# Optimization experiments

Hardware: AMD Instinct MI355X
Metric: run time of the kernel (lower is better)

Reference implementation:

```python
import jax, jax.numpy as jnp
import numpy as np

GAMMA = 0.997
N_STEPS = 5
EPS = 1e-3
Q_WEIGHTS = np.array([1.0, 0.5, 0.0, 2.0], dtype=np.float32)


def _rescale(x):
    # sign(x) * (sqrt(|x|+1) - 1) + eps * x
    return jnp.sign(x) * (jnp.sqrt(jnp.abs(x) + 1.0) - 1.0) + EPS * x


def _inv_rescale(x):
    sign = jnp.sign(x)
    sqrt_arg = 1.0 + 4.0 * EPS * (jnp.abs(x) + 1.0 + EPS)
    square = ((jnp.sqrt(sqrt_arg) - 1.0) / (2.0 * EPS)) ** 2
    return sign * (square - 1.0)


def setup_inputs() -> dict:
    key = jax.random.key(0)
    ks = jax.random.split(key, 6)
    B, T, Q = 4096, 512, 4
    current_q_value = jax.random.normal(ks[0], (B, T, Q), dtype=jnp.float32)
    next_q_value = jax.random.normal(ks[1], (B, T, Q), dtype=jnp.float32)
    log_p = jax.random.normal(ks[2], (B, T), dtype=jnp.float32)
    reward = jax.random.normal(ks[3], (B, T, Q), dtype=jnp.float32)
    is_done = jax.random.bernoulli(ks[4], 0.02, (B, T)).astype(jnp.float32)
    mask = jax.random.bernoulli(ks[5], 0.95, (B, T)).astype(jnp.float32)
    return {
        "current_q_value": current_q_value,
        "next_q_value": next_q_value,
        "log_p": log_p,
        "reward": reward,
        "is_done": is_done,
        "mask": mask,
    }


def reference(current_q_value, next_q_value, log_p, reward, is_done, mask):
    B, T, Q = reward.shape
    q_w = jnp.asarray(Q_WEIGHTS)[None, None, :]                     # (1,1,Q)
    nz = (q_w != 0)
    inv_qw = jnp.where(nz, 1.0 / jnp.where(nz, q_w, 1.0), 0.0)      # (1,1,Q)
    inv_num_q = 1.0 / float((Q_WEIGHTS != 0).sum())

    m = mask[..., None]                                             # (B,T,1)
    d = is_done[..., None]                                          # (B,T,1)

    nq = m * (1.0 - d) * _inv_rescale(next_q_value)                 # (B,T,Q)
    lp = inv_num_q * inv_qw * (m * (1.0 - d) * log_p[..., None])    # (B,T,Q)

    pad = jnp.zeros((B, N_STEPS - 1, Q), dtype=reward.dtype)
    pad_reward = jnp.concatenate([m * reward, pad], axis=1)         # (B,T+n-1,Q)
    lp_pad = jnp.concatenate([lp, pad], axis=1)                     # (B,T+n-1,Q)

    gpow = GAMMA ** jnp.arange(N_STEPS, dtype=jnp.float32)          # gamma^0..gamma^{n-1}
    widx = jnp.arange(T)[:, None] + jnp.arange(N_STEPS)[None, :]    # (T,n) window indices

    reward_sum = jnp.einsum('btnq,n->btq', pad_reward[:, widx, :], gpow)
    log_p_sum = jnp.einsum('btnq,n->btq', lp_pad[:, widx, :], gpow * GAMMA)

    idxs = jnp.minimum(T - 1, jnp.arange(T) + N_STEPS - 1)          # (T,)
    # NOTE: original code uses gamma**idx (absolute index), reproduced faithfully
    next_term = (GAMMA ** idxs.astype(jnp.float32))[None, :, None] * nq[:, idxs, :]

    target = _rescale(reward_sum + next_term + log_p_sum)           # (B,T,Q)
    loss = 0.5 * m * q_w * (current_q_value - target) ** 2
    return loss
```

## Files before the change

kernel.cpp:

```cpp
#include <hip/hip_runtime.h>
#include <math.h>

#define T_DIM 512
#define GAMMA_F 0.997f
#define EPS_F 1e-3f
#define LOG2_GAMMA (-0.0043345907f)

typedef float v4f __attribute__((ext_vector_type(4)));

__device__ __forceinline__ float inv_rescale_f(float x) {
    float s = (x > 0.f) ? 1.f : ((x < 0.f) ? -1.f : 0.f);
    float sqrt_arg = 1.f + 4.f * EPS_F * (fabsf(x) + 1.f + EPS_F);
    float q = (sqrtf(sqrt_arg) - 1.f) * (1.f / (2.f * EPS_F));
    return s * (q * q - 1.f);
}

__device__ __forceinline__ float rescale_f(float x) {
    return copysignf(sqrtf(fabsf(x) + 1.f) - 1.f, x) + EPS_F * x;
}

__global__ __launch_bounds__(256) void nstep_qloss_kernel(
    const float* __restrict__ cur_q,
    const float* __restrict__ next_q,
    const float* __restrict__ log_p,
    const float* __restrict__ reward,
    const float* __restrict__ is_done,
    const float* __restrict__ mask,
    float* __restrict__ out,
    int BT)
{
    int idx = blockIdx.x * 256 + threadIdx.x;
    if (idx >= BT) return;
    int t = idx & (T_DIM - 1);
    int base = idx - t;

    int s1 = (t + 1 < T_DIM) ? t + 1 : T_DIM - 1;
    int s2 = (t + 2 < T_DIM) ? t + 2 : T_DIM - 1;
    int s3 = (t + 3 < T_DIM) ? t + 3 : T_DIM - 1;
    int s4 = (t + 4 < T_DIM) ? t + 4 : T_DIM - 1;
    int o0 = idx;
    int o1 = base + s1, o2 = base + s2, o3 = base + s3, o4 = base + s4;

    const v4f* rew4 = (const v4f*)reward;
    const v4f* nq4  = (const v4f*)next_q;
    const v4f* cq4  = (const v4f*)cur_q;
    v4f* out4       = (v4f*)out;

    float m0 = mask[o0], m1 = mask[o1], m2 = mask[o2], m3 = mask[o3], m4 = mask[o4];
    float d0 = is_done[o0], d1 = is_done[o1], d2 = is_done[o2], d3 = is_done[o3], d4 = is_done[o4];
    float p0 = log_p[o0], p1 = log_p[o1], p2 = log_p[o2], p3 = log_p[o3], p4 = log_p[o4];
    v4f r0 = rew4[o0], r1 = rew4[o1], r2 = rew4[o2], r3 = rew4[o3], r4 = rew4[o4];
    v4f nq = nq4[o4];
    v4f cq = cq4[o0];

    float v1 = (t + 1 < T_DIM) ? 1.f : 0.f;
    float v2 = (t + 2 < T_DIM) ? 1.f : 0.f;
    float v3 = (t + 3 < T_DIM) ? 1.f : 0.f;
    float v4v = (t + 4 < T_DIM) ? 1.f : 0.f;

    const float g1 = GAMMA_F;
    const float g2 = g1 * g1;
    const float g3 = g2 * g1;
    const float g4 = g2 * g2;

    float w0 = m0;
    float w1 = v1 * g1 * m1;
    float w2 = v2 * g2 * m2;
    float w3 = v3 * g3 * m3;
    float w4 = v4v * g4 * m4;

    float a0 = w0 * r0.x; float a1 = w0 * r0.y; float a2 = w0 * r0.z; float a3 = w0 * r0.w;
    a0 = fmaf(w1, r1.x, a0); a1 = fmaf(w1, r1.y, a1); a2 = fmaf(w1, r1.z, a2); a3 = fmaf(w1, r1.w, a3);
    a0 = fmaf(w2, r2.x, a0); a1 = fmaf(w2, r2.y, a1); a2 = fmaf(w2, r2.z, a2); a3 = fmaf(w2, r2.w, a3);
    a0 = fmaf(w3, r3.x, a0); a1 = fmaf(w3, r3.y, a1); a2 = fmaf(w3, r3.z, a2); a3 = fmaf(w3, r3.w, a3);
    a0 = fmaf(w4, r4.x, a0); a1 = fmaf(w4, r4.y, a1); a2 = fmaf(w4, r4.z, a2); a3 = fmaf(w4, r4.w, a3);

    float Ls = w0 * (1.f - d0) * p0;
    Ls = fmaf(w1, (1.f - d1) * p1, Ls);
    Ls = fmaf(w2, (1.f - d2) * p2, Ls);
    Ls = fmaf(w3, (1.f - d3) * p3, Ls);
    Ls = fmaf(w4, (1.f - d4) * p4, Ls);
    Ls *= GAMMA_F * (1.f / 3.f);

    float coeff = exp2f((float)s4 * LOG2_GAMMA);
    float g = coeff * m4 * (1.f - d4);
    float nt0 = g * inv_rescale_f(nq.x);
    float nt1 = g * inv_rescale_f(nq.y);
    float nt2 = g * inv_rescale_f(nq.z);
    float nt3 = g * inv_rescale_f(nq.w);

    float tgt0 = rescale_f(a0 + nt0 + 1.0f * Ls);
    float tgt1 = rescale_f(a1 + nt1 + 2.0f * Ls);
    float tgt2 = rescale_f(a2 + nt2);
    float tgt3 = rescale_f(a3 + nt3 + 0.5f * Ls);

    float hm = 0.5f * m0;
    float e0 = cq.x - tgt0;
    float e1 = cq.y - tgt1;
    float e3 = cq.w - tgt3;
    (void)tgt2;
    v4f o;
    o.x = hm * e0 * e0;
    o.y = hm * 0.5f * e1 * e1;
    o.z = 0.f;
    o.w = hm * 2.0f * e3 * e3;
    out4[idx] = o;
}

extern "C" void kernel_launch(void* const* d_in, const int* in_sizes, int n_in,
                              void* d_out, int out_size, void* d_ws, size_t ws_size,
                              hipStream_t stream) {
    const float* cur_q   = (const float*)d_in[0];
    const float* next_q  = (const float*)d_in[1];
    const float* log_p   = (const float*)d_in[2];
    const float* reward  = (const float*)d_in[3];
    const float* is_done = (const float*)d_in[4];
    const float* mask    = (const float*)d_in[5];
    float* out = (float*)d_out;

    int BT = in_sizes[2];
    int blocks = (BT + 255) / 256;
    hipLaunchKernelGGL(nstep_qloss_kernel, dim3(blocks), dim3(256), 0, stream,
                       cur_q, next_q, log_p, reward, is_done, mask, out, BT);
}
```

Measured before the change: 157.7 us.

## Share n-step window values via wave shuffles and process two elements per thread

Each lane now loads only its own mask, done flag, log_p and reward, then gathers the four following timesteps from neighbouring lanes with shuffle-down instead of issuing five overlapping loads. Waves advance by 60 elements so the last four lanes act as a halo, and each thread handles one element from each half of the flattened B*T range to expose more memory-level parallelism. This is meant to cut redundant global and cache load traffic. In exchange it adds shuffle instructions and about 6% of lanes that compute but never store.

```diff
diff --git a/kernel.cpp b/kernel.cpp
--- a/kernel.cpp
+++ b/kernel.cpp
@@ -27,84 +27,115 @@
     const float* __restrict__ is_done,
     const float* __restrict__ mask,
     float* __restrict__ out,
-    int BT)
+    int HALF)
 {
-    int idx = blockIdx.x * 256 + threadIdx.x;
-    if (idx >= BT) return;
-    int t = idx & (T_DIM - 1);
-    int base = idx - t;
+    int lane = threadIdx.x & 63;
+    int gw   = (blockIdx.x * 256 + threadIdx.x) >> 6;
+    int idx  = gw * 60 + lane;
+    int lidx = (idx < HALF) ? idx : (HALF - 1);
+    bool outv = (lane < 60) && (idx < HALF);
 
-    int s1 = (t + 1 < T_DIM) ? t + 1 : T_DIM - 1;
-    int s2 = (t + 2 < T_DIM) ? t + 2 : T_DIM - 1;
-    int s3 = (t + 3 < T_DIM) ? t + 3 : T_DIM - 1;
-    int s4 = (t + 4 < T_DIM) ? t + 4 : T_DIM - 1;
-    int o0 = idx;
-    int o1 = base + s1, o2 = base + s2, o3 = base + s3, o4 = base + s4;
+    int t    = lidx & (T_DIM - 1);
+    int base = lidx - t;
+    int t4   = (t + 4 < T_DIM) ? (t + 4) : (T_DIM - 1);
+    int o4   = base + t4;
+    int lidx2 = lidx + HALF;
+    int o42   = o4 + HALF;
 
     const v4f* rew4 = (const v4f*)reward;
     const v4f* nq4  = (const v4f*)next_q;
     const v4f* cq4  = (const v4f*)cur_q;
     v4f* out4       = (v4f*)out;
 
-    float m0 = mask[o0], m1 = mask[o1], m2 = mask[o2], m3 = mask[o3], m4 = mask[o4];
-    float d0 = is_done[o0], d1 = is_done[o1], d2 = is_done[o2], d3 = is_done[o3], d4 = is_done[o4];
-    float p0 = log_p[o0], p1 = log_p[o1], p2 = log_p[o2], p3 = log_p[o3], p4 = log_p[o4];
-    v4f r0 = rew4[o0], r1 = rew4[o1], r2 = rew4[o2], r3 = rew4[o3], r4 = rew4[o4];
-    v4f nq = nq4[o4];
-    v4f cq = cq4[o0];
+    float mA = mask[lidx], dA = is_done[lidx], pA = log_p[lidx];
+    v4f   rA = rew4[lidx];
+    float m4A = mask[o4], d4A = is_done[o4];
+    v4f   nqA = nq4[o4], cqA = cq4[lidx];
 
-    float v1 = (t + 1 < T_DIM) ? 1.f : 0.f;
-    float v2 = (t + 2 < T_DIM) ? 1.f : 0.f;
-    float v3 = (t + 3 < T_DIM) ? 1.f : 0.f;
-    float v4v = (t + 4 < T_DIM) ? 1.f : 0.f;
+    float mB = mask[lidx2], dB = is_done[lidx2], pB = log_p[lidx2];
+    v4f   rB = rew4[lidx2];
+    float m4B = mask[o42], d4B = is_done[o42];
+    v4f   nqB = nq4[o42], cqB = cq4[lidx2];
+
+    float LA = mA * (1.f - dA) * pA;
+    float xA = mA * rA.x, yA = mA * rA.y, zA = mA * rA.z, wA = mA * rA.w;
+    float LB = mB * (1.f - dB) * pB;
+    float xB = mB * rB.x, yB = mB * rB.y, zB = mB * rB.z, wB = mB * rB.w;
 
     const float g1 = GAMMA_F;
     const float g2 = g1 * g1;
     const float g3 = g2 * g1;
     const float g4 = g2 * g2;
+    float wk[4];
+    wk[0] = ((t + 1 < T_DIM) ? 1.f : 0.f) * g1;
+    wk[1] = ((t + 2 < T_DIM) ? 1.f : 0.f) * g2;
+    wk[2] = ((t + 3 < T_DIM) ? 1.f : 0.f) * g3;
+    wk[3] = ((t + 4 < T_DIM) ? 1.f : 0.f) * g4;
+    float coeff = exp2f((float)t4 * LOG2_GAMMA);
 
-    float w0 = m0;
-    float w1 = v1 * g1 * m1;
-    float w2 = v2 * g2 * m2;
-    float w3 = v3 * g3 * m3;
-    float w4 = v4v * g4 * m4;
+    float aA0 = xA, aA1 = yA, aA2 = zA, aA3 = wA, LsA = LA;
+    float aB0 = xB, aB1 = yB, aB2 = zB, aB3 = wB, LsB = LB;
+#pragma unroll
+    for (int k = 1; k <= 4; ++k) {
+        float w = wk[k - 1];
+        aA0 = fmaf(w, __shfl_down(xA, k), aA0);
+        aA1 = fmaf(w, __shfl_down(yA, k), aA1);
+        aA2 = fmaf(w, __shfl_down(zA, k), aA2);
+        aA3 = fmaf(w, __shfl_down(wA, k), aA3);
+        LsA = fmaf(w, __shfl_down(LA, k), LsA);
+        aB0 = fmaf(w, __shfl_down(xB, k), aB0);
+        aB1 = fmaf(w, __shfl_down(yB, k), aB1);
+        aB2 = fmaf(w, __shfl_down(zB, k), aB2);
+        aB3 = fmaf(w, __shfl_down(wB, k), aB3);
+        LsB = fmaf(w, __shfl_down(LB, k), LsB);
+    }
+    LsA *= GAMMA_F * (1.f / 3.f);
+    LsB *= GAMMA_F * (1.f / 3.f);
 
-    float a0 = w0 * r0.x; float a1 = w0 * r0.y; float a2 = w0 * r0.z; float a3 = w0 * r0.w;
-    a0 = fmaf(w1, r1.x, a0); a1 = fmaf(w1, r1.y, a1); a2 = fmaf(w1, r1.z, a2); a3 = fmaf(w1, r1.w, a3);
-    a0 = fmaf(w2, r2.x, a0); a1 = fmaf(w2, r2.y, a1); a2 = fmaf(w2, r2.z, a2); a3 = fmaf(w2, r2.w, a3);
-    a0 = fmaf(w3, r3.x, a0); a1 = fmaf(w3, r3.y, a1); a2 = fmaf(w3, r3.z, a2); a3 = fmaf(w3, r3.w, a3);
-    a0 = fmaf(w4, r4.x, a0); a1 = fmaf(w4, r4.y, a1); a2 = fmaf(w4, r4.z, a2); a3 = fmaf(w4, r4.w, a3);
-
-    float Ls = w0 * (1.f - d0) * p0;
-    Ls = fmaf(w1, (1.f - d1) * p1, Ls);
-    Ls = fmaf(w2, (1.f - d2) * p2, Ls);
-    Ls = fmaf(w3, (1.f - d3) * p3, Ls);
-    Ls = fmaf(w4, (1.f - d4) * p4, Ls);
-    Ls *= GAMMA_F * (1.f / 3.f);
-
-    float coeff = exp2f((float)s4 * LOG2_GAMMA);
-    float g = coeff * m4 * (1.f - d4);
-    float nt0 = g * inv_rescale_f(nq.x);
-    float nt1 = g * inv_rescale_f(nq.y);
-    float nt2 = g * inv_rescale_f(nq.z);
-    float nt3 = g * inv_rescale_f(nq.w);
-
-    float tgt0 = rescale_f(a0 + nt0 + 1.0f * Ls);
-    float tgt1 = rescale_f(a1 + nt1 + 2.0f * Ls);
-    float tgt2 = rescale_f(a2 + nt2);
-    float tgt3 = rescale_f(a3 + nt3 + 0.5f * Ls);
-
-    float hm = 0.5f * m0;
-    float e0 = cq.x - tgt0;
-    float e1 = cq.y - tgt1;
-    float e3 = cq.w - tgt3;
-    (void)tgt2;
-    v4f o;
-    o.x = hm * e0 * e0;
-    o.y = hm * 0.5f * e1 * e1;
-    o.z = 0.f;
-    o.w = hm * 2.0f * e3 * e3;
-    out4[idx] = o;
+    {
+        float g = coeff * m4A * (1.f - d4A);
+        float nt0 = g * inv_rescale_f(nqA.x);
+        float nt1 = g * inv_rescale_f(nqA.y);
+        float nt2 = g * inv_rescale_f(nqA.z);
+        float nt3 = g * inv_rescale_f(nqA.w);
+        float tgt0 = rescale_f(aA0 + nt0 + 1.0f * LsA);
+        float tgt1 = rescale_f(aA1 + nt1 + 2.0f * LsA);
+        float tgt2 = rescale_f(aA2 + nt2);
+        float tgt3 = rescale_f(aA3 + nt3 + 0.5f * LsA);
+        (void)tgt2;
+        float hm = 0.5f * mA;
+        float e0 = cqA.x - tgt0;
+        float e1 = cqA.y - tgt1;
+        float e3 = cqA.w - tgt3;
+        v4f o;
+        o.x = hm * e0 * e0;
+        o.y = hm * 0.5f * e1 * e1;
+        o.z = 0.f;
+        o.w = hm * 2.0f * e3 * e3;
+        if (outv) out4[idx] = o;
+    }
+    {
+        float g = coeff * m4B * (1.f - d4B);
+        float nt0 = g * inv_rescale_f(nqB.x);
+        float nt1 = g * inv_rescale_f(nqB.y);
+        float nt2 = g * inv_rescale_f(nqB.z);
+        float nt3 = g * inv_rescale_f(nqB.w);
+        float tgt0 = rescale_f(aB0 + nt0 + 1.0f * LsB);
+        float tgt1 = rescale_f(aB1 + nt1 + 2.0f * LsB);
+        float tgt2 = rescale_f(aB2 + nt2);
+        float tgt3 = rescale_f(aB3 + nt3 + 0.5f * LsB);
+        (void)tgt2;
+        float hm = 0.5f * mB;
+        float e0 = cqB.x - tgt0;
+        float e1 = cqB.y - tgt1;
+        float e3 = cqB.w - tgt3;
+        v4f o;
+        o.x = hm * e0 * e0;
+        o.y = hm * 0.5f * e1 * e1;
+        o.z = 0.f;
+        o.w = hm * 2.0f * e3 * e3;
+        if (outv) out4[idx + HALF] = o;
+    }
 }
 
 extern "C" void kernel_launch(void* const* d_in, const int* in_sizes, int n_in,
@@ -119,7 +150,9 @@
     float* out = (float*)d_out;
 
     int BT = in_sizes[2];
-    int blocks = (BT + 255) / 256;
+    int HALF = BT / 2;
+    int nwaves = (HALF + 59) / 60;
+    int blocks = (nwaves + 3) / 4;
     hipLaunchKernelGGL(nstep_qloss_kernel, dim3(blocks), dim3(256), 0, stream,
-                       cur_q, next_q, log_p, reward, is_done, mask, out, BT);
+                       cur_q, next_q, log_p, reward, is_done, mask, out, HALF);
 }
```

New measurement: 162.0 us. +2.7%, slower.
